# Kernel optimization log

Measured on AMD Instinct MI355X. Metric: run time of the kernel, lower is better.

## Reference

```python
import jax, jax.numpy as jnp
import numpy as np

D_MODEL = 1024
N_HEADS = 16
D_LATENT = 64
LN_EPS = 1e-5


def setup_inputs() -> dict:
    key = jax.random.key(0)
    ks = jax.random.split(key, 9)
    dm, h, dl = D_MODEL, N_HEADS, D_LATENT
    hd = h * dl
    # xavier_uniform with gain=0.1: limit = 0.1 * sqrt(6/(fan_in+fan_out))
    def xavier(k, fan_in, fan_out):
        lim = 0.1 * np.sqrt(6.0 / (fan_in + fan_out))
        return jax.random.uniform(k, (fan_in, fan_out), jnp.float32, -lim, lim)
    return {
        "x": jax.random.normal(ks[0], (4, 2048, dm), jnp.float32),
        "ln_g": jnp.ones((dm,), jnp.float32),
        "ln_b": jnp.zeros((dm,), jnp.float32),
        "wq": xavier(ks[1], dm, hd), "bq": jnp.zeros((hd,), jnp.float32),
        "wk": xavier(ks[2], dm, hd), "bk": jnp.zeros((hd,), jnp.float32),
        "wv": xavier(ks[3], dm, hd), "bv": jnp.zeros((hd,), jnp.float32),
        "wo": xavier(ks[4], hd, dm), "bo": jnp.zeros((dm,), jnp.float32),
    }


def reference(x, ln_g, ln_b, wq, bq, wk, bk, wv, bv, wo, bo):
    b, s, dm = x.shape
    h, dl = N_HEADS, D_LATENT
    # context = raw x (bound before LayerNorm in the torch code)
    context = x
    mu = jnp.mean(x, axis=-1, keepdims=True)
    var = jnp.var(x, axis=-1, keepdims=True)
    xn = (x - mu) * jax.lax.rsqrt(var + LN_EPS) * ln_g + ln_b
    q = (xn @ wq + bq).reshape(b, s, h, dl).transpose(0, 2, 1, 3)          # b h s d
    k = (context @ wk + bk).reshape(b, -1, h, dl).transpose(0, 2, 1, 3)    # b h t d
    v = (context @ wv + bv).reshape(b, -1, h, dl).transpose(0, 2, 1, 3)
    scores = jnp.einsum("bhsd,bhtd->bhst", q, k) / jnp.sqrt(jnp.float32(dl))
    attn = jax.nn.softmax(scores.astype(jnp.float32), axis=-1)
    # dropout omitted (eval mode / deterministic reference)
    out = jnp.einsum("bhst,bhtd->bhsd", attn, v)
    out = out.transpose(0, 2, 1, 3).reshape(b, s, h * dl)
    return out @ wo + bo
```

## Files before the change

### kernel.cpp

```cpp
#include <hip/hip_runtime.h>
#include <cstdint>

typedef __attribute__((ext_vector_type(8))) __bf16 bf16x8;
typedef __attribute__((ext_vector_type(8))) unsigned short u16x8;
typedef __attribute__((ext_vector_type(4))) unsigned short u16x4;
typedef __attribute__((ext_vector_type(4))) float f32x4;
typedef __attribute__((ext_vector_type(2))) unsigned int u32x2;
typedef __attribute__((ext_vector_type(4))) unsigned int u32x4;

__device__ inline unsigned short f2bf(float f) {
  return __builtin_bit_cast(unsigned short, (__bf16)f);
}

__device__ inline void llds16(const void* g, void* l) {
  __builtin_amdgcn_global_load_lds((const uint32_t*)g, (uint32_t*)l, 16, 0, 0);
}

__device__ inline bf16x8 ldfrag(const unsigned short* p) {
  u16x8 v = *(const u16x8*)p;
  return __builtin_bit_cast(bf16x8, v);
}

__device__ inline f32x4 mfma16(bf16x8 a, bf16x8 b, f32x4 c) {
  return __builtin_amdgcn_mfma_f32_16x16x32_bf16(a, b, c, 0, 0, 0);
}

__global__ __launch_bounds__(256) void ln_kernel(
    const float* __restrict__ x, const float* __restrict__ g, const float* __restrict__ be,
    unsigned short* __restrict__ xn, unsigned short* __restrict__ xb)
{
  const int row = blockIdx.x, tid = threadIdx.x;
  const size_t base = (size_t)row * 1024 + tid * 4;
  float4 v = *(const float4*)&x[base];
  float s  = v.x + v.y + v.z + v.w;
  float sq = v.x*v.x + v.y*v.y + v.z*v.z + v.w*v.w;
#pragma unroll
  for (int o = 1; o < 64; o <<= 1) { s += __shfl_xor(s, o); sq += __shfl_xor(sq, o); }
  __shared__ float ls[8];
  if ((tid & 63) == 0) { ls[tid >> 6] = s; ls[4 + (tid >> 6)] = sq; }
  __syncthreads();
  s  = ls[0] + ls[1] + ls[2] + ls[3];
  sq = ls[4] + ls[5] + ls[6] + ls[7];
  const float mu   = s * (1.f / 1024.f);
  const float var  = sq * (1.f / 1024.f) - mu * mu;
  const float rstd = rsqrtf(var + 1e-5f);
  float4 gv = *(const float4*)&g[tid * 4];
  float4 bv = *(const float4*)&be[tid * 4];
  u16x4 a, bb;
  a[0] = f2bf((v.x - mu) * rstd * gv.x + bv.x);
  a[1] = f2bf((v.y - mu) * rstd * gv.y + bv.y);
  a[2] = f2bf((v.z - mu) * rstd * gv.z + bv.z);
  a[3] = f2bf((v.w - mu) * rstd * gv.w + bv.w);
  bb[0] = f2bf(v.x); bb[1] = f2bf(v.y); bb[2] = f2bf(v.z); bb[3] = f2bf(v.w);
  *(u16x4*)&xn[base] = a;
  *(u16x4*)&xb[base] = bb;
}

__global__ __launch_bounds__(256) void wcast_kernel(
    const float* __restrict__ wq, const float* __restrict__ wk,
    const float* __restrict__ wv, const float* __restrict__ wo,
    unsigned short* __restrict__ wT, unsigned short* __restrict__ woT)
{
  __shared__ float t[64][66];
  const int z = blockIdx.z;
  const float* W = (z == 0) ? wq : (z == 1) ? wk : (z == 2) ? wv : wo;
  unsigned short* O = (z < 3) ? (wT + (size_t)z * 1048576) : woT;
  const int n0 = blockIdx.x * 64, k0 = blockIdx.y * 64;
  for (int idx = threadIdx.x; idx < 4096; idx += 256) {
    int r = idx >> 6, c = idx & 63;
    t[r][c] = W[(size_t)(k0 + r) * 1024 + n0 + c];
  }
  __syncthreads();
  for (int idx = threadIdx.x; idx < 4096; idx += 256) {
    int r = idx >> 6, c = idx & 63;
    O[(size_t)(n0 + r) * 1024 + k0 + c] = f2bf(t[c][r]);
  }
}

template<int MODE>
__global__ __launch_bounds__(256) void gemm_kernel(
    const unsigned short* __restrict__ A0, const unsigned short* __restrict__ A1,
    const unsigned short* __restrict__ BT,
    const float* __restrict__ b0, const float* __restrict__ b1, const float* __restrict__ b2,
    void* __restrict__ Cv, int M, int N, int K)
{
  __shared__ unsigned short S[32768];
  const int tid = threadIdx.x;
  const int wave = tid >> 6, lane = tid & 63;
  const int l15 = lane & 15, l4 = lane >> 4;
  const int swz = (l15 & 7) << 3;
  const int NBN = N >> 7;
  const int nwg = gridDim.x, cpx = nwg >> 3;
  const int orig = blockIdx.x;
  const int id = (orig & 7) * cpx + (orig >> 3);
  const int bn = id % NBN, bm = id / NBN;
  const int m0 = bm * 128, n0 = bn * 128;
  const unsigned short* Ap = (MODE == 0 && bn >= 8) ? A1 : A0;
  const int wr = (wave >> 1) * 64, wc = (wave & 1) * 64;

  f32x4 acc[4][4];
#pragma unroll
  for (int m = 0; m < 4; m++)
#pragma unroll
    for (int n = 0; n < 4; n++) acc[m][n] = {0.f, 0.f, 0.f, 0.f};

  auto STAGE = [&](int b, int kt) {
#pragma unroll
    for (int r = 0; r < 4; r++) {
      int D = r * 4096 + tid * 16;
      int row = D >> 7;
      int colus = ((D & 127) >> 1) ^ ((row & 7) << 3);
      llds16(&Ap[(size_t)(m0 + row) * K + kt + colus], &S[b * 16384 + r * 2048 + wave * 512]);
      llds16(&BT[(size_t)(n0 + row) * K + kt + colus],
             &S[b * 16384 + 8192 + r * 2048 + wave * 512]);
    }
  };

  const int KSTEPS = K >> 6;
  int cur = 0;
  STAGE(0, 0);
  for (int ki = 0; ki < KSTEPS; ki++) {
    if (ki < KSTEPS - 1) {
      STAGE(cur ^ 1, (ki + 1) << 6);
      asm volatile("s_waitcnt vmcnt(8)" ::: "memory");
    } else {
      asm volatile("s_waitcnt vmcnt(0)" ::: "memory");
    }
    __builtin_amdgcn_s_barrier();
    __builtin_amdgcn_sched_barrier(0);
    const unsigned short* Asb = &S[cur * 16384];
    const unsigned short* Bsb = &S[cur * 16384 + 8192];
#pragma unroll
    for (int ks = 0; ks < 2; ks++) {
      bf16x8 af[4], bfr[4];
#pragma unroll
      for (int m = 0; m < 4; m++)
        af[m]  = ldfrag(&Asb[(wr + m * 16 + l15) * 64 + ((ks * 32 + l4 * 8) ^ swz)]);
#pragma unroll
      for (int n = 0; n < 4; n++)
        bfr[n] = ldfrag(&Bsb[(wc + n * 16 + l15) * 64 + ((ks * 32 + l4 * 8) ^ swz)]);
#pragma unroll
      for (int m = 0; m < 4; m++)
#pragma unroll
        for (int n = 0; n < 4; n++)
          acc[m][n] = mfma16(af[m], bfr[n], acc[m][n]);
    }
    __builtin_amdgcn_s_barrier();
    cur ^= 1;
  }

#pragma unroll
  for (int nf = 0; nf < 4; nf++) {
    int c = n0 + wc + nf * 16 + l15;
    if (MODE == 0) {
      int sec = c >> 10;
      float bias = (sec == 0 ? b0 : (sec == 1 ? b1 : b2))[c & 1023];
      float sc = (sec == 0) ? 0.18033688011112042f : 1.0f;
      int h = (c >> 6) & 15, d = c & 63;
#pragma unroll
      for (int mf = 0; mf < 4; mf++) {
        int rbase = m0 + wr + mf * 16 + l4 * 4;
        int b = rbase >> 11, t = rbase & 2047;
        if (sec == 2) {
          u16x4 pk;
#pragma unroll
          for (int reg = 0; reg < 4; reg++) pk[reg] = f2bf(acc[mf][nf][reg] + bias);
          *(u16x4*)&((unsigned short*)Cv)[(size_t)2 * 8388608 +
                                          ((size_t)((b * 16 + h) * 64 + d)) * 2048 + t] = pk;
        } else {
#pragma unroll
          for (int reg = 0; reg < 4; reg++) {
            float v = acc[mf][nf][reg] + bias;
            ((unsigned short*)Cv)[(size_t)sec * 8388608 +
                                  ((size_t)(b * 16 + h) * 2048 + t + reg) * 64 + d] =
                f2bf(v * sc);
          }
        }
      }
    } else {
      float bias = b0[c];
#pragma unroll
      for (int mf = 0; mf < 4; mf++) {
#pragma unroll
        for (int reg = 0; reg < 4; reg++) {
          int rrow = m0 + wr + mf * 16 + l4 * 4 + reg;
          ((float*)Cv)[(size_t)rrow * N + c] = acc[mf][nf][reg] + bias;
        }
      }
    }
  }
}

__global__ __launch_bounds__(512, 4) void attn_kernel(
    const unsigned short* __restrict__ Q,
    const unsigned short* __restrict__ Kg,
    const unsigned short* __restrict__ VTg,
    unsigned short* __restrict__ Oa)
{
  __shared__ unsigned short S[32768];
  const int tid = threadIdx.x;
  const int wave = tid >> 6, lane = tid & 63;
  const int l15 = lane & 15, l4 = lane >> 4;
  const int swz = (l15 & 7) << 3;
  const int orig = blockIdx.x;
  const int wg = ((orig & 7) << 6) + (orig >> 3);
  const int qb = wg & 7, bh = wg >> 3;
  const size_t bhbase = (size_t)bh * 131072;
  const int q0 = qb * 256 + wave * 32;

  const u16x8 onesu = {0x3F80, 0x3F80, 0x3F80, 0x3F80, 0x3F80, 0x3F80, 0x3F80, 0x3F80};
  const bf16x8 ones = __builtin_bit_cast(bf16x8, onesu);

  bf16x8 qf[2][2];
#pragma unroll
  for (int m = 0; m < 2; m++)
#pragma unroll
    for (int ks = 0; ks < 2; ks++)
      qf[m][ks] = ldfrag(&Q[bhbase + (size_t)(q0 + m * 16 + l15) * 64 + ks * 32 + l4 * 8]);

  f32x4 accO[2][4];
#pragma unroll
  for (int m = 0; m < 2; m++)
#pragma unroll
    for (int n = 0; n < 4; n++) accO[m][n] = {0.f, 0.f, 0.f, 0.f};
  f32x4 accR[2] = {{0.f, 0.f, 0.f, 0.f}, {0.f, 0.f, 0.f, 0.f}};

  auto STAGE = [&](int b, int jj) {
#pragma unroll
    for (int r = 0; r < 2; r++) {
      int D = r * 8192 + tid * 16;
      int rowK = D >> 7;
      int colKus = ((D & 127) >> 1) ^ ((rowK & 7) << 3);
      llds16(&Kg[bhbase + (size_t)(jj * 128 + rowK) * 64 + colKus],
             &S[b * 16384 + r * 4096 + wave * 512]);
      int rowV = D >> 8;
      int colVus = ((D & 255) >> 1) ^ ((rowV & 7) << 3);
      llds16(&VTg[bhbase + (size_t)rowV * 2048 + jj * 128 + colVus],
             &S[b * 16384 + 8192 + r * 4096 + wave * 512]);
    }
  };

  int cur = 0;
  STAGE(0, 0);
  for (int j = 0; j < 16; j++) {
    if (j < 15) {
      STAGE(cur ^ 1, j + 1);
      asm volatile("s_waitcnt vmcnt(4)" ::: "memory");
    } else {
      asm volatile("s_waitcnt vmcnt(0)" ::: "memory");
    }
    __builtin_amdgcn_s_barrier();
    __builtin_amdgcn_sched_barrier(0);

    const unsigned short* Kb = &S[cur * 16384];
    const unsigned short* Vb = &S[cur * 16384 + 8192];

#pragma unroll
    for (int kt = 0; kt < 4; kt++) {
      bf16x8 kf00 = ldfrag(&Kb[((2 * kt) * 16 + l15) * 64 + ((0 * 32 + l4 * 8) ^ swz)]);
      bf16x8 kf01 = ldfrag(&Kb[((2 * kt) * 16 + l15) * 64 + ((1 * 32 + l4 * 8) ^ swz)]);
      bf16x8 kf10 = ldfrag(&Kb[((2 * kt + 1) * 16 + l15) * 64 + ((0 * 32 + l4 * 8) ^ swz)]);
      bf16x8 kf11 = ldfrag(&Kb[((2 * kt + 1) * 16 + l15) * 64 + ((1 * 32 + l4 * 8) ^ swz)]);
      f32x4 sa = {0.f, 0.f, 0.f, 0.f}, sb = sa, sc = sa, sd = sa;
      __builtin_amdgcn_s_setprio(1);
      sa = mfma16(kf00, qf[0][0], sa); sb = mfma16(kf00, qf[1][0], sb);
      sc = mfma16(kf10, qf[0][0], sc); sd = mfma16(kf10, qf[1][0], sd);
      sa = mfma16(kf01, qf[0][1], sa); sb = mfma16(kf01, qf[1][1], sb);
      sc = mfma16(kf11, qf[0][1], sc); sd = mfma16(kf11, qf[1][1], sd);
      __builtin_amdgcn_s_setprio(0);

      bf16x8 vf[4];
#pragma unroll
      for (int n = 0; n < 4; n++)
        vf[n] = ldfrag(&Vb[(n * 16 + l15) * 128 + ((kt * 32 + l4 * 8) ^ swz)]);

      bf16x8 pf[2];
#pragma unroll
      for (int m = 0; m < 2; m++) {
        const f32x4 se = (m == 0) ? sa : sb;
        const f32x4 so = (m == 0) ? sc : sd;
        uint32_t V0, V1, V2, V3;
        {
          u16x4 pk;
#pragma unroll
          for (int r = 0; r < 4; r++) pk[r] = f2bf(__builtin_amdgcn_exp2f(se[r]));
          u32x2 w = __builtin_bit_cast(u32x2, pk);
          V0 = w[0]; V1 = w[1];
        }
        {
          u16x4 pk;
#pragma unroll
          for (int r = 0; r < 4; r++) pk[r] = f2bf(__builtin_amdgcn_exp2f(so[r]));
          u32x2 w = __builtin_bit_cast(u32x2, pk);
          V2 = w[0]; V3 = w[1];
        }
        asm("s_nop 1\n\t"
            "v_permlane32_swap_b32 %0, %2\n\t"
            "v_permlane32_swap_b32 %1, %3\n\t"
            "v_permlane16_swap_b32 %0, %2\n\t"
            "v_permlane16_swap_b32 %1, %3"
            : "+v"(V0), "+v"(V1), "+v"(V2), "+v"(V3));
        u32x4 fw = {V0, V1, V2, V3};
        pf[m] = __builtin_bit_cast(bf16x8, fw);
      }

      __builtin_amdgcn_s_setprio(1);
#pragma unroll
      for (int m = 0; m < 2; m++) {
        accR[m] = mfma16(pf[m], ones, accR[m]);
#pragma unroll
        for (int n = 0; n < 4; n++)
          accO[m][n] = mfma16(pf[m], vf[n], accO[m][n]);
      }
      __builtin_amdgcn_s_setprio(0);
    }

    __builtin_amdgcn_s_barrier();
    cur ^= 1;
  }

  const int b = bh >> 4, h = bh & 15;
#pragma unroll
  for (int m = 0; m < 2; m++)
#pragma unroll
    for (int reg = 0; reg < 4; reg++) {
      float inv = 1.0f / accR[m][reg];
      int srow = q0 + m * 16 + l4 * 4 + reg;
#pragma unroll
      for (int n = 0; n < 4; n++) {
        float v = accO[m][n][reg] * inv;
        Oa[((size_t)(b * 2048) + srow) * 1024 + h * 64 + n * 16 + l15] = f2bf(v);
      }
    }
}

extern "C" void kernel_launch(void* const* d_in, const int* in_sizes, int n_in,
                              void* d_out, int out_size, void* d_ws, size_t ws_size,
                              hipStream_t stream) {
  (void)in_sizes; (void)n_in; (void)out_size; (void)ws_size;
  const float* x   = (const float*)d_in[0];
  const float* lng = (const float*)d_in[1];
  const float* lnb = (const float*)d_in[2];
  const float* wq  = (const float*)d_in[3];
  const float* bq  = (const float*)d_in[4];
  const float* wk  = (const float*)d_in[5];
  const float* bk  = (const float*)d_in[6];
  const float* wv  = (const float*)d_in[7];
  const float* bv  = (const float*)d_in[8];
  const float* wo  = (const float*)d_in[9];
  const float* bo  = (const float*)d_in[10];

  unsigned short* ws = (unsigned short*)d_ws;
  const size_t NE = 8388608;
  unsigned short* xn  = ws;
  unsigned short* xb  = ws + NE;
  unsigned short* wT  = ws + 2 * NE;
  unsigned short* woT = wT + 3145728;
  unsigned short* qkv = woT + 1048576;
  unsigned short* oat = xb;

  wcast_kernel<<<dim3(16, 16, 4), 256, 0, stream>>>(wq, wk, wv, wo, wT, woT);
  ln_kernel<<<dim3(8192), 256, 0, stream>>>(x, lng, lnb, xn, xb);
  gemm_kernel<0><<<dim3(1536), 256, 0, stream>>>(xn, xb, wT, bq, bk, bv, qkv, 8192, 3072, 1024);
  attn_kernel<<<dim3(512), 512, 0, stream>>>(qkv, qkv + NE, qkv + 2 * NE, oat);
  gemm_kernel<1><<<dim3(512), 256, 0, stream>>>(oat, oat, woT, bo, bo, bo, d_out, 8192, 1024, 1024);
}
```

Measured before the change: 181.7 us.

## Use 256x256-tile 8-wave GEMM for fused QKV projection

Adds a new GEMM kernel for the QKV projection that uses 256x256 output tiles, 512 threads and 128 KB of double-buffered LDS, replacing the 128-wide tile kernel. Each wave computes a 128x64 sub-tile, and the loads for the next K step are split into two halves interleaved with the MFMA phases. The goal is better operand reuse per LDS load and higher arithmetic intensity. The cost is fewer workgroups (384), higher register pressure from 32 accumulators, and large LDS use that limits occupancy.

```diff
diff --git a/kernel.cpp b/kernel.cpp
--- a/kernel.cpp
+++ b/kernel.cpp
@@ -74,6 +74,140 @@
   for (int idx = threadIdx.x; idx < 4096; idx += 256) {
     int r = idx >> 6, c = idx & 63;
     O[(size_t)(n0 + r) * 1024 + k0 + c] = f2bf(t[c][r]);
+  }
+}
+
+__global__ __launch_bounds__(512, 2) void gemm256_kernel(
+    const unsigned short* __restrict__ A0, const unsigned short* __restrict__ A1,
+    const unsigned short* __restrict__ BT,
+    const float* __restrict__ b0, const float* __restrict__ b1, const float* __restrict__ b2,
+    unsigned short* __restrict__ Cv, int M, int N, int K)
+{
+  __shared__ unsigned short S[65536];
+  const int tid = threadIdx.x;
+  const int wave = tid >> 6, lane = tid & 63;
+  const int l15 = lane & 15, l4 = lane >> 4;
+  const int swz = (l15 & 7) << 3;
+  const int NBN = N >> 8;
+  const int nwg = gridDim.x, cpx = nwg >> 3;
+  const int orig = blockIdx.x;
+  const int id = (orig & 7) * cpx + (orig >> 3);
+  const int bn = id % NBN, bm = id / NBN;
+  const int m0 = bm * 256, n0 = bn * 256;
+  const unsigned short* Ap = (bn >= 4) ? A1 : A0;
+  const int wr = (wave >> 2) * 128, wc = (wave & 3) * 64;
+
+  f32x4 acc[8][4];
+#pragma unroll
+  for (int m = 0; m < 8; m++)
+#pragma unroll
+    for (int n = 0; n < 4; n++) acc[m][n] = {0.f, 0.f, 0.f, 0.f};
+
+  auto ISSUE4 = [&](int b, int kt, int half) {
+#pragma unroll
+    for (int r = 0; r < 2; r++) {
+      int rr = half * 2 + r;
+      int D = tid * 16;
+      int row = rr * 64 + (D >> 7);
+      int colus = ((D & 127) >> 1) ^ ((row & 7) << 3);
+      llds16(&Ap[(size_t)(m0 + row) * K + kt + colus],
+             &S[b * 32768 + rr * 4096 + wave * 512]);
+      llds16(&BT[(size_t)(n0 + row) * K + kt + colus],
+             &S[b * 32768 + 16384 + rr * 4096 + wave * 512]);
+    }
+  };
+
+  const int KSTEPS = K >> 6;
+  ISSUE4(0, 0, 0); ISSUE4(0, 0, 1);
+  for (int ki = 0; ki < KSTEPS; ki++) {
+    const int cur = ki & 1;
+    if (ki < KSTEPS - 1) {
+      ISSUE4(cur ^ 1, (ki + 1) << 6, 0);
+      asm volatile("s_waitcnt vmcnt(4)" ::: "memory");
+    } else {
+      asm volatile("s_waitcnt vmcnt(0)" ::: "memory");
+    }
+    __builtin_amdgcn_s_barrier();
+    __builtin_amdgcn_sched_barrier(0);
+    const unsigned short* Asb = &S[cur * 32768];
+    const unsigned short* Bsb = &S[cur * 32768 + 16384];
+
+    bf16x8 bf[4][2];
+#pragma unroll
+    for (int nf = 0; nf < 4; nf++)
+#pragma unroll
+      for (int ks = 0; ks < 2; ks++)
+        bf[nf][ks] = ldfrag(&Bsb[(wc + nf * 16 + l15) * 64 + ((ks * 32 + l4 * 8) ^ swz)]);
+
+#pragma unroll
+    for (int ph = 0; ph < 2; ph++) {
+      bf16x8 af[2][2];
+#pragma unroll
+      for (int i = 0; i < 2; i++)
+#pragma unroll
+        for (int ks = 0; ks < 2; ks++)
+          af[i][ks] =
+              ldfrag(&Asb[(wr + (ph * 2 + i) * 16 + l15) * 64 + ((ks * 32 + l4 * 8) ^ swz)]);
+      __builtin_amdgcn_s_setprio(1);
+#pragma unroll
+      for (int ks = 0; ks < 2; ks++)
+#pragma unroll
+        for (int i = 0; i < 2; i++)
+#pragma unroll
+          for (int nf = 0; nf < 4; nf++)
+            acc[ph * 2 + i][nf] = mfma16(af[i][ks], bf[nf][ks], acc[ph * 2 + i][nf]);
+      __builtin_amdgcn_s_setprio(0);
+    }
+
+    if (ki < KSTEPS - 1) ISSUE4(cur ^ 1, (ki + 1) << 6, 1);
+
+#pragma unroll
+    for (int ph = 2; ph < 4; ph++) {
+      bf16x8 af[2][2];
+#pragma unroll
+      for (int i = 0; i < 2; i++)
+#pragma unroll
+        for (int ks = 0; ks < 2; ks++)
+          af[i][ks] =
+              ldfrag(&Asb[(wr + (ph * 2 + i) * 16 + l15) * 64 + ((ks * 32 + l4 * 8) ^ swz)]);
+      __builtin_amdgcn_s_setprio(1);
+#pragma unroll
+      for (int ks = 0; ks < 2; ks++)
+#pragma unroll
+        for (int i = 0; i < 2; i++)
+#pragma unroll
+          for (int nf = 0; nf < 4; nf++)
+            acc[ph * 2 + i][nf] = mfma16(af[i][ks], bf[nf][ks], acc[ph * 2 + i][nf]);
+      __builtin_amdgcn_s_setprio(0);
+    }
+    __builtin_amdgcn_s_barrier();
+  }
+
+#pragma unroll
+  for (int nf = 0; nf < 4; nf++) {
+    int c = n0 + wc + nf * 16 + l15;
+    int sec = c >> 10;
+    float bias = (sec == 0 ? b0 : (sec == 1 ? b1 : b2))[c & 1023];
+    float sc = (sec == 0) ? 0.18033688011112042f : 1.0f;
+    int h = (c >> 6) & 15, d = c & 63;
+#pragma unroll
+    for (int mf = 0; mf < 8; mf++) {
+      int rbase = m0 + wr + mf * 16 + l4 * 4;
+      int b = rbase >> 11, t = rbase & 2047;
+      if (sec == 2) {
+        u16x4 pk;
+#pragma unroll
+        for (int reg = 0; reg < 4; reg++) pk[reg] = f2bf(acc[mf][nf][reg] + bias);
+        *(u16x4*)&Cv[(size_t)2 * 8388608 + ((size_t)((b * 16 + h) * 64 + d)) * 2048 + t] = pk;
+      } else {
+#pragma unroll
+        for (int reg = 0; reg < 4; reg++) {
+          float v = acc[mf][nf][reg] + bias;
+          Cv[(size_t)sec * 8388608 + ((size_t)(b * 16 + h) * 2048 + t + reg) * 64 + d] =
+              f2bf(v * sc);
+        }
+      }
+    }
   }
 }
 
@@ -361,7 +495,7 @@
 
   wcast_kernel<<<dim3(16, 16, 4), 256, 0, stream>>>(wq, wk, wv, wo, wT, woT);
   ln_kernel<<<dim3(8192), 256, 0, stream>>>(x, lng, lnb, xn, xb);
-  gemm_kernel<0><<<dim3(1536), 256, 0, stream>>>(xn, xb, wT, bq, bk, bv, qkv, 8192, 3072, 1024);
+  gemm256_kernel<<<dim3(384), 512, 0, stream>>>(xn, xb, wT, bq, bk, bv, qkv, 8192, 3072, 1024);
   attn_kernel<<<dim3(512), 512, 0, stream>>>(qkv, qkv + NE, qkv + 2 * NE, oat);
   gemm_kernel<1><<<dim3(512), 256, 0, stream>>>(oat, oat, woT, bo, bo, bo, d_out, 8192, 1024, 1024);
 }
```

After: 186.2 us. 2.5% more time.
